# Performance work log

Hardware: AMD Instinct MI355X
Metric: run time of the kernel (lower is better)

Reference implementation:

```python
import jax, jax.numpy as jnp
import numpy as np

B, K, D, E = 8192, 5, 128, 128
QD = D + 1              # query_dim = embedding_dimension + time_encoding_dim(=1)
KD = K * (D + E + 1)    # flattened neighborhood feature width = key_dim*5


def setup_inputs() -> dict:
    key = jax.random.key(0)
    ks = jax.random.split(key, 20)
    n = jax.random.normal
    u = jax.random.uniform
    return {
        # hop-2 neighborhood (neighbors-of-neighbors of B roots)
        "emb0": n(ks[0], (B * K, K, D), jnp.float32),
        "ef0": n(ks[1], (B * K, K, E), jnp.float32),
        "td0": u(ks[2], (B * K, K, 1), jnp.float32),
        # hop-1 neighborhood
        "emb1": n(ks[3], (B, K, D), jnp.float32),
        "ef1": n(ks[4], (B, K, E), jnp.float32),
        "td1": u(ks[5], (B, K, 1), jnp.float32),
        # root embeddings
        "emb2": n(ks[6], (B, D), jnp.float32),
        # single-head MultiheadAttention params (q/k/v in-proj + out-proj)
        "Wq": n(ks[7], (QD, QD), jnp.float32) * 0.05,
        "bq": jnp.zeros((QD,), jnp.float32),
        "Wk": n(ks[8], (QD, KD), jnp.float32) * 0.02,
        "bk": jnp.zeros((QD,), jnp.float32),
        "Wv": n(ks[9], (QD, KD), jnp.float32) * 0.02,
        "bv": jnp.zeros((QD,), jnp.float32),
        "Wo": n(ks[10], (QD, QD), jnp.float32) * 0.05,
        "bo": jnp.zeros((QD,), jnp.float32),
        # fc1: (query_dim + D) -> D, fc2: D -> D
        "W1": n(ks[11], (D, QD + D), jnp.float32) * 0.05,
        "b1": jnp.zeros((D,), jnp.float32),
        "W2": n(ks[12], (D, D), jnp.float32) * 0.05,
        "b2": jnp.zeros((D,), jnp.float32),
    }


def reference(emb0, ef0, td0, emb1, ef1, td1, emb2,
              Wq, bq, Wk, bk, Wv, bv, Wo, bo, W1, b1, W2, b2):
    def attn(q, kv):
        # single-head MHA, batch_first; PyTorch scales q by head_dim**-0.5
        qp = (q @ Wq.T + bq) * (1.0 / jnp.sqrt(jnp.asarray(QD, q.dtype)))
        kp = kv @ Wk.T + bk
        vp = kv @ Wv.T + bv
        w = jax.nn.softmax(jnp.einsum("bqd,bkd->bqk", qp, kp), axis=-1)
        o = jnp.einsum("bqk,bkd->bqd", w, vp)
        return o @ Wo.T + bo

    def mlp(x):
        return jax.nn.relu(x @ W1.T + b1) @ W2.T + b2

    # i = 0: hop-2 neighborhoods attend into hop-1 nodes
    nf0 = jnp.concatenate([emb0, ef0, td0], axis=-1).reshape(B, K, KD)  # [B,K,KD]
    q0 = jnp.concatenate([emb1, td1], axis=-1)                          # [B,K,QD]
    a0 = attn(q0, nf0)
    r0 = mlp(jnp.concatenate([a0, emb1], axis=-1))                      # [B,K,D]

    # i = 1 (last): hop-1 neighborhoods; 2-D root query is reshaped to [1,B,QD]
    # so attention runs across the whole batch, as in the original code.
    nf1 = jnp.concatenate([emb1, ef1, td1], axis=-1).reshape(1, B, KD)  # [1,B,KD]
    q1 = jnp.concatenate([emb2, jnp.zeros((B, 1), emb2.dtype)], axis=-1)[None]
    a1 = attn(q1, nf1)
    r1 = mlp(jnp.concatenate([a1, emb2[None]], axis=-1))[0]             # [B,D]

    return (r0, r1)
```

## Files before the change

kernel.cpp:

```cpp
#include <hip/hip_runtime.h>

#define B_   8192
#define K_   5
#define D_   128
#define QD_  129
#define KD_  1285
#define SQ_  132
#define BK_  40960
#define QPAD 160
#define VPAD 144
#define KDP  1312

typedef unsigned short u16;
typedef unsigned int   u32;
typedef __attribute__((ext_vector_type(8))) short bf8_t;
typedef __attribute__((ext_vector_type(4))) float f4_t;
typedef __attribute__((address_space(3))) u32 lds_u32;
typedef __attribute__((address_space(1))) const u32 glob_u32;

#define MFMA16(a, b, c) __builtin_amdgcn_mfma_f32_16x16x32_bf16(a, b, c, 0, 0, 0)

__device__ __forceinline__ u16 f2bf(float x) {
  u32 u = __float_as_uint(x);
  u = (u + 0x7fffu + ((u >> 16) & 1u)) >> 16;
  return (u16)u;
}
__device__ __forceinline__ u32 pack2(float a, float b) {
  return (u32)f2bf(a) | ((u32)f2bf(b) << 16);
}
__device__ __forceinline__ float exp2_fast(float x) {
#if __has_builtin(__builtin_amdgcn_exp2f)
  return __builtin_amdgcn_exp2f(x);
#else
  float r; asm("v_exp_f32 %0, %1" : "=v"(r) : "v"(x)); return r;
#endif
}
__device__ __forceinline__ u32 cvtpk(float a, float b) {
  u32 r;
  asm("v_cvt_pk_bf16_f32 %0, %1, %2" : "=v"(r) : "v"(a), "v"(b));
  return r;
}
__device__ __forceinline__ int swz8(int row, int seg) {
  return (row << 5) + (((seg ^ (row >> 1)) & 3) << 3);
}
__device__ __forceinline__ void gload16(const u16* src, u16* ldsdst) {
  __builtin_amdgcn_global_load_lds((glob_u32*)src, (lds_u32*)ldsdst, 16, 0, 0);
}
#define WAIT_VM0() asm volatile("s_waitcnt vmcnt(0)" ::: "memory")
#define WAIT_VM3() asm volatile("s_waitcnt vmcnt(3)" ::: "memory")
#define WAIT_VM4() asm volatile("s_waitcnt vmcnt(4)" ::: "memory")
#define WAIT_VM6() asm volatile("s_waitcnt vmcnt(6)" ::: "memory")
#define WAIT_LGKM0() asm volatile("s_waitcnt lgkmcnt(0)" ::: "memory")

__global__ __launch_bounds__(256) void convw_k(
    const float* __restrict__ Wq, const float* __restrict__ Wk,
    const float* __restrict__ Wv, const float* __restrict__ Wo,
    const float* __restrict__ W1, const float* __restrict__ W2,
    u16* __restrict__ wb)
{
  int idx = blockIdx.x * 256 + threadIdx.x;
  if (idx < 377856) {
    int r = idx / KDP, c = idx - r * KDP;
    float v = 0.f;
    if (c < KD_) {
      if (r < 129) v = Wk[r * KD_ + c];
      else if (r < 258) v = Wv[(r - 129) * KD_ + c];
    }
    wb[idx] = f2bf(v);
    return;
  }
  int i2 = idx - 377856;
  if (i2 < 23040) {
    int r = i2 / 160, c = i2 - r * 160;
    wb[idx] = f2bf((r < 129 && c < 129) ? Wq[r * 129 + c] : 0.f);
    return;
  }
  i2 -= 23040;
  if (i2 < 23040) {
    int r = i2 / 160, c = i2 - r * 160;
    wb[idx] = f2bf((r < 129 && c < 129) ? Wo[r * 129 + c] : 0.f);
    return;
  }
  i2 -= 23040;
  if (i2 < 41472) {
    int r = i2 / 288, c = i2 - r * 288;
    wb[idx] = f2bf((r < 128 && c < 257) ? W1[r * 257 + c] : 0.f);
    return;
  }
  i2 -= 41472;
  if (i2 < 18432) {
    int r = i2 / 128, c = i2 - r * 128;
    wb[idx] = f2bf(r < 128 ? W2[r * 128 + c] : 0.f);
  }
}

__global__ __launch_bounds__(256) void packnf_k(
    const float* __restrict__ emb, const float* __restrict__ ef,
    const float* __restrict__ td, u16* __restrict__ dst, int nofs, int rows)
{
  int idx = blockIdx.x * 256 + threadIdx.x;
  if (idx >= rows * 328) return;
  int nr = idx / 328, q = idx - nr * 328;
  const int n = nofs + nr;
  const int c0 = q * 4;
  u16 o[4];
#pragma unroll
  for (int i = 0; i < 4; ++i) {
    int c = c0 + i;
    float v = 0.f;
    if (c < KD_) {
      int j = c / 257, r = c - j * 257;
      int base = (n * 5 + j) << 7;
      v = (r < 128) ? emb[base + r] : (r < 256) ? ef[base + r - 128] : td[n * 5 + j];
    }
    o[i] = f2bf(v);
  }
  *(uint2*)&dst[(size_t)nr * KDP + c0] = *(const uint2*)o;
}

template<int GA, bool RELU, int OM0, int OM1, bool DUAL>
__global__ __launch_bounds__(256) void gmm_k(
    int nK, int Kw, int nch,
    const void* __restrict__ A, int ast,
    const float* __restrict__ g1, const float* __restrict__ g2,
    const u16* __restrict__ Wb,
    const float* __restrict__ b0, void* __restrict__ out0, int ost0, int N0,
    const float* __restrict__ b1, void* __restrict__ out1, int ost1,
    float scale)
{
  __shared__ u16 Ws_[3][9 * 512];
  const int t = threadIdx.x, lane = t & 63, w = t >> 6;
  const int lrow = lane & 15, lk = lane >> 4;
  const int bid = blockIdx.x;
  const int x = bid / nch, colh = bid - x * nch;
  const int n0 = x * 64;
  const int colofs = colh * 144;
  const int drow = lane >> 2, dseg = lane & 3;
  const int arow = n0 + w * 16 + lrow;

  f4_t acc[9];
#pragma unroll
  for (int ct = 0; ct < 9; ++ct) acc[ct] = (f4_t){0.f, 0.f, 0.f, 0.f};

  bf8_t afE, afO;
  float rE[8], rO[8];

  auto issueR = [&](int kst, float (&r)[8]) {
    const int cb = kst * 32 + lk * 8;
#pragma unroll
    for (int i = 0; i < 8; ++i) {
      int c = cb + i;
      uintptr_t pa = (uintptr_t)((const float*)A + (arow << 7) + c);
      uintptr_t pt = (uintptr_t)(g2 ? (g2 + arow) : (const float*)A);
      uintptr_t sel = (c < 128) ? pa : pt;
      float v = *(const float*)sel;
      r[i] = (c < 128) ? v : ((c == 128 && g2) ? v : 0.f);
    }
  };
  auto cvt8 = [&](const float (&r)[8]) -> bf8_t {
    union { bf8_t v; u32 u[4]; } xx;
#pragma unroll
    for (int i = 0; i < 4; ++i) xx.u[i] = pack2(r[2 * i], r[2 * i + 1]);
    return xx.v;
  };
  auto loadAf = [&](int kst) -> bf8_t {
    return *(const bf8_t*)((const u16*)A + (size_t)arow * ast + kst * 32 + lk * 8);
  };
  auto dmaW = [&](int kst, u16* wbuf) {
    const int c0 = kst * 32;
#pragma unroll
    for (int si = 0; si < 3; ++si) {
      int s = w + si * 4;
      if (s < 9) {
        int rr = colofs + s * 16 + drow;
        int sseg = (dseg ^ (rr >> 1)) & 3;
        gload16(&Wb[(size_t)rr * Kw + c0 + sseg * 8], wbuf + s * 512);
      }
    }
  };
  auto compute = [&](bf8_t af, const u16* wsb) {
#pragma unroll
    for (int ct = 0; ct < 9; ++ct) {
      bf8_t bf = *(const bf8_t*)&wsb[swz8(ct * 16 + lrow, lk)];
      acc[ct] = MFMA16(af, bf, acc[ct]);
    }
  };

  if constexpr (GA == 0) {
    u16 *wa = Ws_[0], *wbuf = Ws_[1], *wc = Ws_[2];
    afE = loadAf(0);
    dmaW(0, wa);
    if (nK > 1) { afO = loadAf(1); dmaW(1, wbuf); }
    if (nK > 1) { WAIT_VM4(); } else { WAIT_VM0(); }
    __builtin_amdgcn_s_barrier();
    int k = 0;
    while (true) {
      if (k + 2 < nK) dmaW(k + 2, wc);
      compute(afE, wa);
      if (k + 2 < nK) afE = loadAf(k + 2);
      if (k + 1 >= nK) break;
      if (k + 2 < nK) { WAIT_VM4(); } else { WAIT_VM0(); }
      __builtin_amdgcn_s_barrier();
      { u16* tp = wa; wa = wbuf; wbuf = wc; wc = tp; }
      ++k;
      if (k + 2 < nK) dmaW(k + 2, wc);
      compute(afO, wa);
      if (k + 2 < nK) afO = loadAf(k + 2);
      if (k + 1 >= nK) break;
      if (k + 2 < nK) { WAIT_VM4(); } else { WAIT_VM0(); }
      __builtin_amdgcn_s_barrier();
      { u16* tp = wa; wa = wbuf; wbuf = wc; wc = tp; }
      ++k;
    }
  } else {
    issueR(0, rE);
    dmaW(0, Ws_[0]);
    WAIT_VM0();
    afE = cvt8(rE);
    __builtin_amdgcn_s_barrier();
    int cur = 0, k = 0;
    while (true) {
      if (k + 1 < nK) { issueR(k + 1, rO); dmaW(k + 1, Ws_[cur ^ 1]); }
      compute(afE, Ws_[cur]);
      if (k + 1 >= nK) break;
      WAIT_VM0();
      afO = cvt8(rO);
      __builtin_amdgcn_s_barrier();
      cur ^= 1; ++k;
      if (k + 1 < nK) { issueR(k + 1, rE); dmaW(k + 1, Ws_[cur ^ 1]); }
      compute(afO, Ws_[cur]);
      if (k + 1 >= nK) break;
      WAIT_VM0();
      afE = cvt8(rE);
      __builtin_amdgcn_s_barrier();
      cur ^= 1; ++k;
    }
  }

#pragma unroll
  for (int ct = 0; ct < 9; ++ct) {
    const int col = colofs + ct * 16 + lrow;
#pragma unroll
    for (int r = 0; r < 4; ++r) {
      const int n = n0 + w * 16 + lk * 4 + r;
      float v = acc[ct][r];
      if (col < N0) {
        v = (v + b0[col]) * scale;
        if (RELU) v = fmaxf(v, 0.f);
        if (OM0 == 0)      ((float*)out0)[(size_t)n * ost0 + col] = v;
        else if (OM0 == 1) ((u16*)out0)[(size_t)n * ost0 + col] = f2bf(v);
        else               ((u16*)out0)[(size_t)col * ost0 + n] = f2bf(v);
      } else if (DUAL) {
        int o = col - N0;
        if (o < 129) {
          v = (v + b1[o]) * scale;
          if (RELU) v = fmaxf(v, 0.f);
          if (OM1 == 0)      ((float*)out1)[(size_t)n * ost1 + o] = v;
          else if (OM1 == 1) ((u16*)out1)[(size_t)n * ost1 + o] = f2bf(v);
          else               ((u16*)out1)[(size_t)o * ost1 + n] = f2bf(v);
        }
      }
    }
  }
}

__global__ __launch_bounds__(256) void embpack_k(
    const float* __restrict__ src, u16* __restrict__ dst, int rows)
{
  int idx = blockIdx.x * 256 + threadIdx.x;
  if (idx >= rows * 128) return;
  int n = idx >> 7, c = idx & 127;
  dst[(size_t)n * 288 + 129 + c] = f2bf(src[idx]);
}

__global__ __launch_bounds__(256) void attn0_k(
    const float* __restrict__ qp, const float* __restrict__ kp,
    const float* __restrict__ vp, u16* __restrict__ o0b)
{
  __shared__ float qs[4][5][SQ_], ks[4][5][SQ_], vs[4][5][SQ_];
  __shared__ float ps[4][5][8];
  const int t = threadIdx.x;
  const int bbase = blockIdx.x * 4;
  for (int idx = t; idx < 4 * 5 * SQ_; idx += 256) {
    int bl = idx / (5 * SQ_);
    int rem = idx - bl * 5 * SQ_;
    int row = rem / SQ_;
    int d = rem - row * SQ_;
    int n = (bbase + bl) * 5 + row;
    float qv = 0.f, kv = 0.f, vv = 0.f;
    if (d < QD_) { qv = qp[n * SQ_ + d]; kv = kp[n * SQ_ + d]; vv = vp[n * SQ_ + d]; }
    qs[bl][row][d] = qv; ks[bl][row][d] = kv; vs[bl][row][d] = vv;
  }
  __syncthreads();
  const int w = t >> 6, lane = t & 63;
  if (lane < 25) {
    int qq = lane / 5, kk = lane - (lane / 5) * 5;
    float s = 0.f;
    for (int c = 0; c < QD_; ++c) s += qs[w][qq][c] * ks[w][kk][c];
    ps[w][qq][kk] = s;
  }
  __syncthreads();
  if (lane < 5) {
    float m = -1e30f;
#pragma unroll
    for (int k = 0; k < 5; ++k) m = fmaxf(m, ps[w][lane][k]);
    float l = 0.f; float e[5];
#pragma unroll
    for (int k = 0; k < 5; ++k) { e[k] = __expf(ps[w][lane][k] - m); l += e[k]; }
    float inv = 1.f / l;
#pragma unroll
    for (int k = 0; k < 5; ++k) ps[w][lane][k] = e[k] * inv;
  }
  __syncthreads();
  for (int d = lane; d < 160; d += 64) {
#pragma unroll
    for (int qq = 0; qq < 5; ++qq) {
      float o = 0.f;
      if (d < QD_) {
#pragma unroll
        for (int k = 0; k < 5; ++k) o += ps[w][qq][k] * vs[w][k][d];
      }
      o0b[(size_t)((bbase + w) * 5 + qq) * 160 + d] = f2bf(o);
    }
  }
}

#define QB   128
#define KVB  64
#define NSPLIT 8
#define NT   ((B_ / NSPLIT) / KVB)
__global__ __launch_bounds__(512, 4) void flashm_k(
    const u16* __restrict__ qp, const u16* __restrict__ kp,
    const u16* __restrict__ vpT, float* __restrict__ oacc,
    float* __restrict__ marr, float* __restrict__ larr)
{
  __shared__ u16 Ks[2][5 * 2048];
  __shared__ u16 Vs[2 * 4608];
  __shared__ u16 Ps[2 * 4096];
  const int t = threadIdx.x, lane = t & 63, w = t >> 6;
  const int lrow = lane & 15, lk = lane >> 4;
  const int split = blockIdx.x & (NSPLIT - 1);
  const int q0 = (blockIdx.x >> 3) * QB;
  const int drow = lane >> 2, dseg = lane & 3;
  const int kbase = split * (B_ / NSPLIT);

  auto dmaK = [&](int k0, u16* kb) {
#pragma unroll
    for (int si = 0; si < 3; ++si) {
      int s = w + si * 8;
      if (s >= 20) s -= 20;
      int kst = s >> 2, rg = s & 3;
      int r = rg * 16 + drow;
      int sseg = (dseg ^ (r >> 1)) & 3;
      gload16(&kp[(size_t)(k0 + r) * QPAD + kst * 32 + sseg * 8],
              kb + kst * 2048 + rg * 512);
    }
  };
  auto dmaV = [&](int k0) {
#pragma unroll
    for (int si = 0; si < 3; ++si) {
      int s = w + si * 8;
      if (s >= 18) s -= 18;
      int kst = (s >= 9) ? 1 : 0;
      int rg = s - kst * 9;
      int r = rg * 16 + drow;
      int sseg = (dseg ^ (r >> 1)) & 3;
      gload16(&vpT[(size_t)r * B_ + k0 + kst * 32 + sseg * 8],
              Vs + kst * 4608 + rg * 512);
    }
  };

  bf8_t qf[5];
  {
    const u16* qrow = qp + (size_t)(q0 + w * 16 + lrow) * QPAD;
#pragma unroll
    for (int kst = 0; kst < 5; ++kst)
      qf[kst] = *(const bf8_t*)(qrow + kst * 32 + lk * 8);
  }

  f4_t acc[9];
#pragma unroll
  for (int ct = 0; ct < 9; ++ct) acc[ct] = (f4_t){0.f, 0.f, 0.f, 0.f};
  float m_[4] = {-1e30f, -1e30f, -1e30f, -1e30f};
  float l_[4] = {0.f, 0.f, 0.f, 0.f};

  dmaK(kbase, Ks[0]);
  for (int tl = 0; tl < NT; ++tl) {
    const int k0 = kbase + tl * KVB;
    const int cur = tl & 1;
    dmaV(k0);
    const bool more = (tl + 1 < NT);
    if (more) dmaK(k0 + KVB, Ks[cur ^ 1]);
    if (more) { WAIT_VM6(); } else { WAIT_VM3(); }
    __builtin_amdgcn_s_barrier();

    f4_t s4[4];
#pragma unroll
    for (int ct = 0; ct < 4; ++ct) s4[ct] = (f4_t){0.f, 0.f, 0.f, 0.f};
#pragma unroll
    for (int kst = 0; kst < 5; ++kst) {
#pragma unroll
      for (int ct = 0; ct < 4; ++ct) {
        bf8_t b = *(const bf8_t*)&Ks[cur][kst * 2048 + swz8(ct * 16 + lrow, lk)];
        s4[ct] = MFMA16(qf[kst], b, s4[ct]);
      }
    }

    float pm[4];
#pragma unroll
    for (int r = 0; r < 4; ++r) {
      pm[r] = fmaxf(fmaxf(s4[0][r], s4[1][r]), fmaxf(s4[2][r], s4[3][r]));
#pragma unroll
      for (int mk = 1; mk <= 8; mk <<= 1) pm[r] = fmaxf(pm[r], __shfl_xor(pm[r], mk));
    }
    bool need = false;
#pragma unroll
    for (int r = 0; r < 4; ++r) need = need || (pm[r] > m_[r] + 8.f);
    if (__any(need)) {
      float cf[4];
#pragma unroll
      for (int r = 0; r < 4; ++r) {
        float mn = fmaxf(m_[r], pm[r]);
        cf[r] = exp2_fast(m_[r] - mn);
        m_[r] = mn;
        l_[r] *= cf[r];
      }
#pragma unroll
      for (int ct = 0; ct < 9; ++ct) {
#pragma unroll
        for (int r = 0; r < 4; ++r) acc[ct][r] *= cf[r];
      }
    }
    float pv[4][4];
    float rs[4] = {0.f, 0.f, 0.f, 0.f};
#pragma unroll
    for (int ct = 0; ct < 4; ++ct) {
#pragma unroll
      for (int r = 0; r < 4; ++r) {
        pv[ct][r] = exp2_fast(s4[ct][r] - m_[r]);
        rs[r] += pv[ct][r];
      }
    }
#pragma unroll
    for (int half = 0; half < 2; ++half) {
#pragma unroll
      for (int r = 0; r < 4; ++r) {
        u32 pk = cvtpk(pv[half * 2][r], pv[half * 2 + 1][r]);
        const int q = w * 16 + lk * 4 + r;
        const int c0 = lrow, c1 = 16 + lrow;
        const int base = half * 4096 + (q << 5);
        Ps[base + ((((c0 >> 3) ^ (q >> 1)) & 3) << 3) + (c0 & 7)] = (u16)pk;
        Ps[base + ((((c1 >> 3) ^ (q >> 1)) & 3) << 3) + (c1 & 7)] = (u16)(pk >> 16);
      }
    }
#pragma unroll
    for (int r = 0; r < 4; ++r) {
#pragma unroll
      for (int mk = 1; mk <= 8; mk <<= 1) rs[r] += __shfl_xor(rs[r], mk);
      l_[r] += rs[r];
    }
    WAIT_LGKM0();
    __builtin_amdgcn_sched_barrier(0);

    if (more) { WAIT_VM3(); } else { WAIT_VM0(); }
    __builtin_amdgcn_s_barrier();

#pragma unroll
    for (int kst = 0; kst < 2; ++kst) {
      bf8_t a = *(const bf8_t*)&Ps[kst * 4096 + swz8(w * 16 + lrow, lk)];
#pragma unroll
      for (int ct = 0; ct < 9; ++ct) {
        bf8_t b = *(const bf8_t*)&Vs[kst * 4608 + swz8(ct * 16 + lrow, lk)];
        acc[ct] = MFMA16(a, b, acc[ct]);
      }
    }
    __builtin_amdgcn_s_barrier();
  }

#pragma unroll
  for (int ct = 0; ct < 9; ++ct) {
    const int col = ct * 16 + lrow;
    if (col < SQ_) {
#pragma unroll
      for (int r = 0; r < 4; ++r)
        oacc[((size_t)split * B_ + q0 + w * 16 + lk * 4 + r) * SQ_ + col] = acc[ct][r];
    }
  }
  if (lrow == 0) {
#pragma unroll
    for (int r = 0; r < 4; ++r) {
      size_t i = (size_t)split * B_ + q0 + w * 16 + lk * 4 + r;
      marr[i] = m_[r];
      larr[i] = l_[r];
    }
  }
}

__global__ __launch_bounds__(256) void combine_k(
    const float* __restrict__ oacc, const float* __restrict__ marr,
    const float* __restrict__ larr, u16* __restrict__ o1b)
{
  int idx = blockIdx.x * 256 + threadIdx.x;
  if (idx >= B_ * 160) return;
  int n = idx / 160, d = idx - n * 160;
  float v = 0.f;
  if (d < QD_) {
    float m = -1e30f;
#pragma unroll
    for (int s = 0; s < NSPLIT; ++s) m = fmaxf(m, marr[s * B_ + n]);
    float l = 0.f, o = 0.f;
#pragma unroll
    for (int s = 0; s < NSPLIT; ++s) {
      float e = exp2_fast(marr[s * B_ + n] - m);
      l += larr[s * B_ + n] * e;
      o += oacc[((size_t)s * B_ + n) * SQ_ + d] * e;
    }
    v = o / l;
  }
  o1b[idx] = f2bf(v);
}

extern "C" void kernel_launch(void* const* d_in, const int* in_sizes, int n_in,
                              void* d_out, int out_size, void* d_ws, size_t ws_size,
                              hipStream_t stream)
{
  const float* emb0 = (const float*)d_in[0];
  const float* ef0  = (const float*)d_in[1];
  const float* td0  = (const float*)d_in[2];
  const float* emb1 = (const float*)d_in[3];
  const float* ef1  = (const float*)d_in[4];
  const float* td1  = (const float*)d_in[5];
  const float* emb2 = (const float*)d_in[6];
  const float* Wq = (const float*)d_in[7];  const float* bq = (const float*)d_in[8];
  const float* Wk = (const float*)d_in[9];  const float* bk = (const float*)d_in[10];
  const float* Wv = (const float*)d_in[11]; const float* bv = (const float*)d_in[12];
  const float* Wo = (const float*)d_in[13]; const float* bo = (const float*)d_in[14];
  const float* W1 = (const float*)d_in[15]; const float* b1 = (const float*)d_in[16];
  const float* W2 = (const float*)d_in[17]; const float* b2 = (const float*)d_in[18];
  float* out = (float*)d_out;

  char* ws = (char*)d_ws;
  u16* wb   = (u16*)ws;
  u16* wkv  = wb;
  u16* wq_b = wb + 377856;
  u16* wo_b = wb + 400896;
  u16* w1_b = wb + 423936;
  u16* w2_b = wb + 465408;
  float* kp0 = (float*)(ws + 1048576);
  float* vp0 = (float*)(ws + 22675456);
  u16*   nfp = (u16*)(ws + 44302336);
  float* qp0 = (float*)(ws + 44302336);
  u16*   o0b = (u16*)(ws + 65929216);
  u16*   cat0= (u16*)(ws + 1048576);
  u16*   h0  = (u16*)(ws + 24641536);
  u16*   nf1p = (u16*)(ws + 1048576);
  u16*   qp1b = (u16*)(ws + 22675456);
  u16*   kp1b = (u16*)(ws + 25296896);
  u16*   vp1T = (u16*)(ws + 27918336);
  u16*   o1b  = (u16*)(ws + 30277632);
  float* marr = (float*)(ws + 32899072);
  float* larr = (float*)(ws + 33161216);
  u16*   cat1 = (u16*)(ws + 33423360);
  u16*   h1   = (u16*)(ws + 38141952);
  float* oacc = (float*)(ws + 40239104);

  const float scale = 0.08804509063256238f;
  const float scale2 = scale * 1.4426950408889634f;
  const int HROWS = 20480;

  convw_k<<<1890, 256, 0, stream>>>(Wq, Wk, Wv, Wo, W1, W2, wb);

  for (int h = 0; h < 2; ++h) {
    packnf_k<<<(HROWS * 328 + 255) / 256, 256, 0, stream>>>(
        emb0, ef0, td0, nfp, h * HROWS, HROWS);
    gmm_k<0, false, 0, 0, true><<<(HROWS / 64) * 2, 256, 0, stream>>>(
        41, KDP, 2, nfp, KDP, nullptr, nullptr, wkv,
        bk, kp0 + (size_t)h * HROWS * SQ_, SQ_, QD_,
        bv, vp0 + (size_t)h * HROWS * SQ_, SQ_, 1.f);
  }
  gmm_k<1, false, 0, 0, false><<<640, 256, 0, stream>>>(
      5, 160, 1, emb1, 0, nullptr, td1, wq_b,
      bq, qp0, SQ_, QD_, nullptr, nullptr, 0, scale);
  attn0_k<<<B_ / 4, 256, 0, stream>>>(qp0, kp0, vp0, o0b);
  hipMemsetAsync(cat0, 0, 23592960, stream);
  embpack_k<<<(BK_ * 128 + 255) / 256, 256, 0, stream>>>(emb1, cat0, BK_);
  gmm_k<0, false, 1, 0, false><<<640, 256, 0, stream>>>(
      5, 160, 1, o0b, 160, nullptr, nullptr, wo_b,
      bo, cat0, 288, QD_, nullptr, nullptr, 0, 1.f);
  gmm_k<0, true, 1, 0, false><<<640, 256, 0, stream>>>(
      9, 288, 1, cat0, 288, nullptr, nullptr, w1_b,
      b1, h0, 128, 128, nullptr, nullptr, 0, 1.f);
  gmm_k<0, false, 0, 0, false><<<640, 256, 0, stream>>>(
      4, 128, 1, h0, 128, nullptr, nullptr, w2_b,
      b2, out, 128, 128, nullptr, nullptr, 0, 1.f);

  packnf_k<<<(B_ * 328 + 255) / 256, 256, 0, stream>>>(
      emb1, ef1, td1, nf1p, 0, B_);
  hipMemsetAsync(qp1b, 0, 2621440, stream);
  hipMemsetAsync(kp1b, 0, 2621440, stream);
  hipMemsetAsync(vp1T, 0, 2359296, stream);
  gmm_k<0, false, 1, 2, true><<<(B_ / 64) * 2, 256, 0, stream>>>(
      41, KDP, 2, nf1p, KDP, nullptr, nullptr, wkv,
      bk, kp1b, QPAD, QD_, bv, vp1T, B_, 1.f);
  gmm_k<1, false, 1, 0, false><<<128, 256, 0, stream>>>(
      5, 160, 1, emb2, 0, nullptr, nullptr, wq_b,
      bq, qp1b, QPAD, QD_, nullptr, nullptr, 0, scale2);
  flashm_k<<<(B_ / QB) * NSPLIT, 512, 0, stream>>>(qp1b, kp1b, vp1T, oacc, marr, larr);
  combine_k<<<(B_ * 160 + 255) / 256, 256, 0, stream>>>(oacc, marr, larr, o1b);
  hipMemsetAsync(cat1, 0, 4718592, stream);
  embpack_k<<<(B_ * 128 + 255) / 256, 256, 0, stream>>>(emb2, cat1, B_);
  gmm_k<0, false, 1, 0, false><<<128, 256, 0, stream>>>(
      5, 160, 1, o1b, 160, nullptr, nullptr, wo_b,
      bo, cat1, 288, QD_, nullptr, nullptr, 0, 1.f);
  gmm_k<0, true, 1, 0, false><<<128, 256, 0, stream>>>(
      9, 288, 1, cat1, 288, nullptr, nullptr, w1_b,
      b1, h1, 128, 128, nullptr, nullptr, 0, 1.f);
  gmm_k<0, false, 0, 0, false><<<128, 256, 0, stream>>>(
      4, 128, 1, h1, 128, nullptr, nullptr, w2_b,
      b2, out + (size_t)BK_ * D_, 128, 128, nullptr, nullptr, 0, 1.f);
}
```

Before: 438.5 us.

## Store hop-2 q/k/v projections in bf16 and defer flash row-sum reduction

The hop-2 query, key and value projections are now written as bf16 with a 160-wide row stride instead of fp32 with a 132-wide stride. attn0_k reads them with vectorized 8-byte loads and computes its dot products with float4 LDS reads. This roughly halves the intermediate traffic between the projection GEMMs and the small attention kernel. Separately, the flash-attention loop now shuffle-reduces the row max only when a rescale is needed and sums the row totals once after the loop, removing shuffles from each tile. The cost is reduced intermediate precision, and the rescale check now uses per-lane maxima.

```diff
diff --git a/kernel.cpp b/kernel.cpp
--- a/kernel.cpp
+++ b/kernel.cpp
@@ -24,6 +24,9 @@
   u32 u = __float_as_uint(x);
   u = (u + 0x7fffu + ((u >> 16) & 1u)) >> 16;
   return (u16)u;
+}
+__device__ __forceinline__ float bf2f(u16 v) {
+  return __uint_as_float((u32)v << 16);
 }
 __device__ __forceinline__ u32 pack2(float a, float b) {
   return (u32)f2bf(a) | ((u32)f2bf(b) << 16);
@@ -274,29 +277,45 @@
 }
 
 __global__ __launch_bounds__(256) void attn0_k(
-    const float* __restrict__ qp, const float* __restrict__ kp,
-    const float* __restrict__ vp, u16* __restrict__ o0b)
+    const u16* __restrict__ qp, const u16* __restrict__ kp,
+    const u16* __restrict__ vp, u16* __restrict__ o0b)
 {
   __shared__ float qs[4][5][SQ_], ks[4][5][SQ_], vs[4][5][SQ_];
   __shared__ float ps[4][5][8];
   const int t = threadIdx.x;
   const int bbase = blockIdx.x * 4;
-  for (int idx = t; idx < 4 * 5 * SQ_; idx += 256) {
-    int bl = idx / (5 * SQ_);
-    int rem = idx - bl * 5 * SQ_;
-    int row = rem / SQ_;
-    int d = rem - row * SQ_;
+  for (int idx = t; idx < 4 * 5 * 33; idx += 256) {
+    int bl = idx / 165;
+    int rem = idx - bl * 165;
+    int row = rem / 33;
+    int g = rem - row * 33;
     int n = (bbase + bl) * 5 + row;
-    float qv = 0.f, kv = 0.f, vv = 0.f;
-    if (d < QD_) { qv = qp[n * SQ_ + d]; kv = kp[n * SQ_ + d]; vv = vp[n * SQ_ + d]; }
-    qs[bl][row][d] = qv; ks[bl][row][d] = kv; vs[bl][row][d] = vv;
+    int d0 = g * 4;
+    uint2 uq = *(const uint2*)&qp[(size_t)n * 160 + d0];
+    uint2 uk = *(const uint2*)&kp[(size_t)n * 160 + d0];
+    uint2 uv = *(const uint2*)&vp[(size_t)n * 160 + d0];
+    u16 eq[4] = {(u16)uq.x, (u16)(uq.x >> 16), (u16)uq.y, (u16)(uq.y >> 16)};
+    u16 ek[4] = {(u16)uk.x, (u16)(uk.x >> 16), (u16)uk.y, (u16)(uk.y >> 16)};
+    u16 ev[4] = {(u16)uv.x, (u16)(uv.x >> 16), (u16)uv.y, (u16)(uv.y >> 16)};
+#pragma unroll
+    for (int i = 0; i < 4; ++i) {
+      int d = d0 + i;
+      bool ok = d < QD_;
+      qs[bl][row][d] = ok ? bf2f(eq[i]) : 0.f;
+      ks[bl][row][d] = ok ? bf2f(ek[i]) : 0.f;
+      vs[bl][row][d] = ok ? bf2f(ev[i]) : 0.f;
+    }
   }
   __syncthreads();
   const int w = t >> 6, lane = t & 63;
   if (lane < 25) {
     int qq = lane / 5, kk = lane - (lane / 5) * 5;
     float s = 0.f;
-    for (int c = 0; c < QD_; ++c) s += qs[w][qq][c] * ks[w][kk][c];
+    for (int c = 0; c < SQ_; c += 4) {
+      float4 qv = *(const float4*)&qs[w][qq][c];
+      float4 kv = *(const float4*)&ks[w][kk][c];
+      s += qv.x * kv.x + qv.y * kv.y + qv.z * kv.z + qv.w * kv.w;
+    }
     ps[w][qq][kk] = s;
   }
   __syncthreads();
@@ -406,21 +425,20 @@
       }
     }
 
-    float pm[4];
-#pragma unroll
-    for (int r = 0; r < 4; ++r) {
-      pm[r] = fmaxf(fmaxf(s4[0][r], s4[1][r]), fmaxf(s4[2][r], s4[3][r]));
-#pragma unroll
-      for (int mk = 1; mk <= 8; mk <<= 1) pm[r] = fmaxf(pm[r], __shfl_xor(pm[r], mk));
-    }
-    bool need = false;
-#pragma unroll
-    for (int r = 0; r < 4; ++r) need = need || (pm[r] > m_[r] + 8.f);
+    float lmax[4];
+#pragma unroll
+    for (int r = 0; r < 4; ++r)
+      lmax[r] = fmaxf(fmaxf(s4[0][r], s4[1][r]), fmaxf(s4[2][r], s4[3][r]));
+    bool need = (lmax[0] > m_[0] + 8.f) || (lmax[1] > m_[1] + 8.f) ||
+                (lmax[2] > m_[2] + 8.f) || (lmax[3] > m_[3] + 8.f);
     if (__any(need)) {
       float cf[4];
 #pragma unroll
       for (int r = 0; r < 4; ++r) {
-        float mn = fmaxf(m_[r], pm[r]);
+        float pm = lmax[r];
+#pragma unroll
+        for (int mk = 1; mk <= 8; mk <<= 1) pm = fmaxf(pm, __shfl_xor(pm, mk));
+        float mn = fmaxf(m_[r], pm);
         cf[r] = exp2_fast(m_[r] - mn);
         m_[r] = mn;
         l_[r] *= cf[r];
@@ -432,13 +450,12 @@
       }
     }
     float pv[4][4];
-    float rs[4] = {0.f, 0.f, 0.f, 0.f};
 #pragma unroll
     for (int ct = 0; ct < 4; ++ct) {
 #pragma unroll
       for (int r = 0; r < 4; ++r) {
         pv[ct][r] = exp2_fast(s4[ct][r] - m_[r]);
-        rs[r] += pv[ct][r];
+        l_[r] += pv[ct][r];
       }
     }
 #pragma unroll
@@ -453,12 +470,6 @@
         Ps[base + ((((c1 >> 3) ^ (q >> 1)) & 3) << 3) + (c1 & 7)] = (u16)(pk >> 16);
       }
     }
-#pragma unroll
-    for (int r = 0; r < 4; ++r) {
-#pragma unroll
-      for (int mk = 1; mk <= 8; mk <<= 1) rs[r] += __shfl_xor(rs[r], mk);
-      l_[r] += rs[r];
-    }
     WAIT_LGKM0();
     __builtin_amdgcn_sched_barrier(0);
 
@@ -475,6 +486,12 @@
       }
     }
     __builtin_amdgcn_s_barrier();
+  }
+
+#pragma unroll
+  for (int r = 0; r < 4; ++r) {
+#pragma unroll
+    for (int mk = 1; mk <= 8; mk <<= 1) l_[r] += __shfl_xor(l_[r], mk);
   }
 
 #pragma unroll
@@ -546,13 +563,13 @@
   u16* wo_b = wb + 400896;
   u16* w1_b = wb + 423936;
   u16* w2_b = wb + 465408;
-  float* kp0 = (float*)(ws + 1048576);
-  float* vp0 = (float*)(ws + 22675456);
-  u16*   nfp = (u16*)(ws + 44302336);
-  float* qp0 = (float*)(ws + 44302336);
-  u16*   o0b = (u16*)(ws + 65929216);
-  u16*   cat0= (u16*)(ws + 1048576);
-  u16*   h0  = (u16*)(ws + 24641536);
+  u16*   kp0b = (u16*)(ws + 1048576);
+  u16*   vp0b = (u16*)(ws + 14155776);
+  u16*   qp0b = (u16*)(ws + 27262976);
+  u16*   nfp  = (u16*)(ws + 44302336);
+  u16*   o0b  = (u16*)(ws + 65929216);
+  u16*   cat0 = (u16*)(ws + 1048576);
+  u16*   h0   = (u16*)(ws + 24641536);
   u16*   nf1p = (u16*)(ws + 1048576);
   u16*   qp1b = (u16*)(ws + 22675456);
   u16*   kp1b = (u16*)(ws + 25296896);
@@ -573,15 +590,15 @@
   for (int h = 0; h < 2; ++h) {
     packnf_k<<<(HROWS * 328 + 255) / 256, 256, 0, stream>>>(
         emb0, ef0, td0, nfp, h * HROWS, HROWS);
-    gmm_k<0, false, 0, 0, true><<<(HROWS / 64) * 2, 256, 0, stream>>>(
+    gmm_k<0, false, 1, 1, true><<<(HROWS / 64) * 2, 256, 0, stream>>>(
         41, KDP, 2, nfp, KDP, nullptr, nullptr, wkv,
-        bk, kp0 + (size_t)h * HROWS * SQ_, SQ_, QD_,
-        bv, vp0 + (size_t)h * HROWS * SQ_, SQ_, 1.f);
-  }
-  gmm_k<1, false, 0, 0, false><<<640, 256, 0, stream>>>(
+        bk, kp0b + (size_t)h * HROWS * 160, 160, QD_,
+        bv, vp0b + (size_t)h * HROWS * 160, 160, 1.f);
+  }
+  gmm_k<1, false, 1, 0, false><<<640, 256, 0, stream>>>(
       5, 160, 1, emb1, 0, nullptr, td1, wq_b,
-      bq, qp0, SQ_, QD_, nullptr, nullptr, 0, scale);
-  attn0_k<<<B_ / 4, 256, 0, stream>>>(qp0, kp0, vp0, o0b);
+      bq, qp0b, 160, QD_, nullptr, nullptr, 0, scale);
+  attn0_k<<<B_ / 4, 256, 0, stream>>>(qp0b, kp0b, vp0b, o0b);
   hipMemsetAsync(cat0, 0, 23592960, stream);
   embpack_k<<<(BK_ * 128 + 255) / 256, 256, 0, stream>>>(emb1, cat0, BK_);
   gmm_k<0, false, 1, 0, false><<<640, 256, 0, stream>>>(
```

Result: faster. 416.2 us (-5.1%).
